# Optimization experiments

Measured on AMD Instinct MI355X. Metric: run time of the kernel, lower is better.

Reference implementation:

```python
import jax, jax.numpy as jnp
import numpy as np

T_HORIZON, S_DIM, A_DIM, H = 65536, 128, 8, 256
GAMMA, LMBDA, EPS_CLIP, VF_COEF, ENT_COEF = 0.99, 0.95, 0.2, 0.5, 0.01
LOG2PI = float(np.log(2.0 * np.pi))


def setup_inputs() -> dict:
    key = jax.random.key(0)
    ks = jax.random.split(key, 24)
    s = jax.random.normal(ks[0], (T_HORIZON, S_DIM), jnp.float32)
    a = jax.random.normal(ks[1], (T_HORIZON, A_DIM), jnp.float32)
    r = jax.random.normal(ks[2], (T_HORIZON, 1), jnp.float32)
    sp = jax.random.normal(ks[3], (T_HORIZON, S_DIM), jnp.float32)
    log_prob_a_old = jax.random.normal(ks[4], (T_HORIZON, 1), jnp.float32)
    d_mask = (jax.random.uniform(ks[5], (T_HORIZON, 1)) > 0.05).astype(jnp.float32)

    def lin(k, fan_in, fan_out, std):
        return jax.random.normal(k, (fan_in, fan_out), jnp.float32) * (std / np.sqrt(fan_in))

    params = dict(
        pi_W1=lin(ks[6], S_DIM, H, np.sqrt(2)), pi_b1=jnp.zeros((H,), jnp.float32),
        pi_W2=lin(ks[7], H, H, np.sqrt(2)),     pi_b2=jnp.zeros((H,), jnp.float32),
        mu_W=lin(ks[8], H, A_DIM, 0.01),        mu_b=jnp.zeros((A_DIM,), jnp.float32),
        log_std=jnp.zeros((A_DIM,), jnp.float32),
        v_W1=lin(ks[9], S_DIM, H, np.sqrt(2)),  v_b1=jnp.zeros((H,), jnp.float32),
        v_W2=lin(ks[10], H, H, np.sqrt(2)),     v_b2=jnp.zeros((H,), jnp.float32),
        vh_W=lin(ks[11], H, 1, 1.0),            vh_b=jnp.zeros((1,), jnp.float32),
    )
    return dict(s=s, a=a, r=r, sp=sp, log_prob_a_old=log_prob_a_old, d_mask=d_mask, **params)


def reference(s, a, r, sp, log_prob_a_old, d_mask,
              pi_W1, pi_b1, pi_W2, pi_b2, mu_W, mu_b, log_std,
              v_W1, v_b1, v_W2, v_b2, vh_W, vh_b):
    def mlp(x, W1, b1, W2, b2):
        return jnp.tanh(jnp.tanh(x @ W1 + b1) @ W2 + b2)

    def v_fn(x):
        return mlp(x, v_W1, v_b1, v_W2, v_b2) @ vh_W + vh_b  # [N, 1]

    # ---- GAE (computed under no_grad in the original) ----
    values = jax.lax.stop_gradient(v_fn(s))                  # [T, 1]
    v_last = jax.lax.stop_gradient(v_fn(sp[-1:]))            # [1, 1]
    next_values = jnp.concatenate([values[1:], v_last], axis=0)
    deltas = r + GAMMA * next_values * d_mask - values       # [T, 1]

    def gae_step(gae, inp):
        delta, m = inp
        gae = delta + GAMMA * LMBDA * m * gae
        return gae, gae

    _, advantages = jax.lax.scan(gae_step, jnp.zeros((1,), deltas.dtype),
                                 (deltas, d_mask), reverse=True)  # [T, 1]
    returns = advantages + values
    advantages = (advantages - advantages.mean()) / (advantages.std(ddof=1) + 1e-8)
    advantages = jax.lax.stop_gradient(advantages)
    returns = jax.lax.stop_gradient(returns)

    # ---- PPO clipped loss (single full-batch pass) ----
    mu = mlp(s, pi_W1, pi_b1, pi_W2, pi_b2) @ mu_W + mu_b    # [T, A]
    std = jnp.exp(log_std)
    log_prob = (-0.5 * ((a - mu) / std) ** 2 - log_std - 0.5 * LOG2PI).sum(-1, keepdims=True)
    ratio = jnp.exp(log_prob - log_prob_a_old)               # [T, 1]
    pg_loss = -jnp.minimum(ratio * advantages,
                           jnp.clip(ratio, 1.0 - EPS_CLIP, 1.0 + EPS_CLIP) * advantages).mean()
    diff = v_fn(s) - returns
    vf_loss = jnp.where(jnp.abs(diff) < 1.0, 0.5 * diff ** 2, jnp.abs(diff) - 0.5).mean()
    entropy = (0.5 + 0.5 * LOG2PI + log_std).mean()          # Normal entropy, constant over batch
    return pg_loss + VF_COEF * vf_loss - ENT_COEF * entropy
```

## Files before the change

kernel.cpp:

```cpp
#include <hip/hip_runtime.h>
#include <math.h>

#define TH 65536
#define SD 128
#define AD 8
#define HD 256

constexpr float GAMMA  = 0.99f;
constexpr float LMBDA  = 0.95f;
constexpr float EPSC   = 0.2f;
constexpr float VFC    = 0.5f;
constexpr float ENTC   = 0.01f;
constexpr float LOG2PI = 1.8378770664093453f;

typedef _Float16 half8 __attribute__((ext_vector_type(8)));
typedef __fp16 fp16x2 __attribute__((ext_vector_type(2)));
typedef __attribute__((ext_vector_type(4))) float f32x4;

constexpr size_t WS_VALUES = 0;
constexpr size_t WS_RATIO  = 131080;
constexpr size_t WS_CHP    = 196616;
constexpr size_t WS_CHB    = 196680;
constexpr size_t WS_SCAL   = 196744;
constexpr size_t WS_BF     = 196752;
constexpr size_t SW_PIW1 = 0;
constexpr size_t SW_PIW2 = 32768;
constexpr size_t SW_VW1  = 98304;
constexpr size_t SW_VW2  = 131072;

__device__ __forceinline__ unsigned pk2h(float a, float b) {
    fp16x2 h = __builtin_amdgcn_cvt_pkrtz(a, b);
    return __builtin_bit_cast(unsigned, h);
}

__device__ __forceinline__ float ftanh(float x) {
    float e = __expf(x + x);
    return fmaf(-2.f, __builtin_amdgcn_rcpf(e + 1.f), 1.f);
}

__device__ __forceinline__ float atomLoad(const float* p) {
    return __hip_atomic_load(p, __ATOMIC_RELAXED, __HIP_MEMORY_SCOPE_AGENT);
}

__global__ __launch_bounds__(256) void swizzle_kernel(
    const float* __restrict__ piW1, const float* __restrict__ vW1,
    const float* __restrict__ piW2, const float* __restrict__ vW2,
    unsigned short* __restrict__ dPiW1, unsigned short* __restrict__ dVW1,
    unsigned short* __restrict__ dPiW2, unsigned short* __restrict__ dVW2,
    float* __restrict__ scal)
{
    if (blockIdx.x == 0 && threadIdx.x < 8) scal[threadIdx.x] = 0.f;
    int g = blockIdx.x * 256 + threadIdx.x;
    const float* S; unsigned short* D; int lo;
    if      (g <  8192) { S = piW1; D = dPiW1; lo = 0;     }
    else if (g < 24576) { S = piW2; D = dPiW2; lo = 8192;  }
    else if (g < 32768) { S = vW1;  D = dVW1;  lo = 24576; }
    else                { S = vW2;  D = dVW2;  lo = 32768; }
    int q = g - lo;
    int k = q >> 6, n4 = (q & 63) * 4;
    float4 v = *(const float4*)(S + (size_t)k * HD + n4);
    int ks = k >> 5, kq = (k >> 3) & 3, j = k & 7;
    int nt = n4 >> 4, nr = n4 & 15;
    unsigned short* base = D + ((size_t)(ks * 16 + nt) * 64 + kq * 16 + nr) * 8 + j;
    unsigned p01 = pk2h(v.x, v.y);
    unsigned p23 = pk2h(v.z, v.w);
    base[0]  = (unsigned short)(p01 & 0xffff);
    base[8]  = (unsigned short)(p01 >> 16);
    base[16] = (unsigned short)(p23 & 0xffff);
    base[24] = (unsigned short)(p23 >> 16);
}

__device__ __forceinline__ void runlayer1(
    f32x4* acc, const unsigned short* __restrict__ Ws,
    const half8* afr, int colhalf, int lane)
{
    const half8* Wp = (const half8*)Ws + (size_t)(colhalf * 8) * 64 + lane;
    half8 b[2][8];
#pragma unroll
    for (int nt = 0; nt < 8; ++nt) acc[nt] = (f32x4){0.f, 0.f, 0.f, 0.f};
#pragma unroll
    for (int nt = 0; nt < 8; ++nt) b[0][nt] = Wp[(0 * 16 + nt) * 64];
#pragma unroll
    for (int nt = 0; nt < 8; ++nt) b[1][nt] = Wp[(1 * 16 + nt) * 64];
#pragma unroll
    for (int ks = 0; ks < 4; ++ks) {
        const int cur = ks & 1;
#pragma unroll
        for (int nt = 0; nt < 8; ++nt)
            acc[nt] = __builtin_amdgcn_mfma_f32_16x16x32_f16(afr[ks], b[cur][nt], acc[nt], 0, 0, 0);
        if (ks < 2) {
#pragma unroll
            for (int nt = 0; nt < 8; ++nt) b[cur][nt] = Wp[((ks + 2) * 16 + nt) * 64];
        }
    }
}

__device__ __forceinline__ void runlayer2(
    f32x4* acc, const unsigned short* __restrict__ Ws,
    const unsigned short* h1, int l15, int quad, int rowgrp, int colhalf, int lane)
{
    const half8* Wp = (const half8*)Ws + (size_t)(colhalf * 8) * 64 + lane;
    const unsigned short* Ap = h1 + (rowgrp * 16 + l15) * 264 + quad * 8;
    half8 b[2][8];
    half8 af[2];
#pragma unroll
    for (int nt = 0; nt < 8; ++nt) acc[nt] = (f32x4){0.f, 0.f, 0.f, 0.f};
    af[0] = *(const half8*)(Ap + 0 * 32);
#pragma unroll
    for (int nt = 0; nt < 8; ++nt) b[0][nt] = Wp[(0 * 16 + nt) * 64];
    af[1] = *(const half8*)(Ap + 1 * 32);
#pragma unroll
    for (int nt = 0; nt < 8; ++nt) b[1][nt] = Wp[(1 * 16 + nt) * 64];
#pragma unroll
    for (int ks = 0; ks < 8; ++ks) {
        const int cur = ks & 1;
#pragma unroll
        for (int nt = 0; nt < 8; ++nt)
            acc[nt] = __builtin_amdgcn_mfma_f32_16x16x32_f16(af[cur], b[cur][nt], acc[nt], 0, 0, 0);
        if (ks < 6) {
            af[cur] = *(const half8*)(Ap + (ks + 2) * 32);
#pragma unroll
            for (int nt = 0; nt < 8; ++nt) b[cur][nt] = Wp[((ks + 2) * 16 + nt) * 64];
        }
    }
}

__device__ __forceinline__ void store4(unsigned short* dst, int stride,
                                       float t0, float t1, float t2, float t3)
{
    unsigned p01 = pk2h(t0, t1), p23 = pk2h(t2, t3);
    dst[0]          = (unsigned short)(p01 & 0xffff);
    dst[stride]     = (unsigned short)(p01 >> 16);
    dst[2 * stride] = (unsigned short)(p23 & 0xffff);
    dst[3 * stride] = (unsigned short)(p23 >> 16);
}

__global__ __launch_bounds__(256, 3) void mlp_fused_kernel(
    const float* __restrict__ X, const float* __restrict__ Xlast,
    const unsigned short* __restrict__ piW1s, const float* __restrict__ pib1,
    const unsigned short* __restrict__ piW2s, const float* __restrict__ pib2,
    const float* __restrict__ muW, const float* __restrict__ mub,
    const float* __restrict__ logstd,
    const float* __restrict__ act, const float* __restrict__ lpold,
    const unsigned short* __restrict__ vW1s, const float* __restrict__ vb1,
    const unsigned short* __restrict__ vW2s, const float* __restrict__ vb2,
    const float* __restrict__ vhW, const float* __restrict__ vhb,
    float* __restrict__ values, float* __restrict__ ratio)
{
    __shared__ unsigned short h1[32 * 264];
    __shared__ float cmb[32 * 8];
    __shared__ float val[32];
    const int tid = threadIdx.x;
    const int lane = tid & 63, wave = tid >> 6;
    const int l15 = lane & 15, quad = lane >> 4;
    const int rowgrp = wave >> 1, colhalf = wave & 1;
    const bool vonly = (blockIdx.x == gridDim.x - 1);
    const float* Xp = vonly ? Xlast : X + (size_t)blockIdx.x * 32 * SD;
    const int nrows = vonly ? 1 : 32;
    const int vout0 = vonly ? TH : blockIdx.x * 32;

    if (tid < 32) val[tid] = 0.f;
    cmb[tid] = 0.f;

    const int rr = rowgrp * 16 + l15;
    const float* xrow = Xp + (size_t)(rr < nrows ? rr : 0) * SD;
    half8 afr[4];
#pragma unroll
    for (int ks = 0; ks < 4; ++ks) {
        float4 v0 = *(const float4*)(xrow + ks * 32 + quad * 8);
        float4 v1 = *(const float4*)(xrow + ks * 32 + quad * 8 + 4);
        if (rr >= nrows) { v0 = make_float4(0.f, 0.f, 0.f, 0.f); v1 = v0; }
        uint4 u = make_uint4(pk2h(v0.x, v0.y), pk2h(v0.z, v0.w),
                             pk2h(v1.x, v1.y), pk2h(v1.z, v1.w));
        afr[ks] = __builtin_bit_cast(half8, u);
    }

    f32x4 acc[8];

    if (!vonly) {
        runlayer1(acc, piW1s, afr, colhalf, lane);
#pragma unroll
        for (int ntl = 0; ntl < 8; ++ntl) {
            int col = (colhalf * 8 + ntl) * 16 + l15;
            float bb = pib1[col];
            store4(&h1[(rowgrp * 16 + quad * 4) * 264 + col], 264,
                   ftanh(acc[ntl][0] + bb), ftanh(acc[ntl][1] + bb),
                   ftanh(acc[ntl][2] + bb), ftanh(acc[ntl][3] + bb));
        }
        __syncthreads();
        runlayer2(acc, piW2s, h1, l15, quad, rowgrp, colhalf, lane);
        float pm[4][8];
#pragma unroll
        for (int rg = 0; rg < 4; ++rg)
#pragma unroll
            for (int aj = 0; aj < 8; ++aj) pm[rg][aj] = 0.f;
#pragma unroll
        for (int ntl = 0; ntl < 8; ++ntl) {
            int col = (colhalf * 8 + ntl) * 16 + l15;
            float bb = pib2[col];
            float4 w0 = *(const float4*)(muW + (size_t)col * AD);
            float4 w1 = *(const float4*)(muW + (size_t)col * AD + 4);
            float wv[8] = {w0.x, w0.y, w0.z, w0.w, w1.x, w1.y, w1.z, w1.w};
#pragma unroll
            for (int rg = 0; rg < 4; ++rg) {
                float hv = ftanh(acc[ntl][rg] + bb);
#pragma unroll
                for (int aj = 0; aj < 8; ++aj) pm[rg][aj] = fmaf(hv, wv[aj], pm[rg][aj]);
            }
        }
#pragma unroll
        for (int off = 8; off >= 1; off >>= 1)
#pragma unroll
            for (int rg = 0; rg < 4; ++rg)
#pragma unroll
                for (int aj = 0; aj < 8; ++aj)
                    pm[rg][aj] += __shfl_xor(pm[rg][aj], off, 16);
        if (l15 == 0) {
#pragma unroll
            for (int rg = 0; rg < 4; ++rg) {
                int rowi = rowgrp * 16 + quad * 4 + rg;
#pragma unroll
                for (int aj = 0; aj < 8; ++aj)
                    atomicAdd(&cmb[rowi * 8 + aj], pm[rg][aj]);
            }
        }
        __syncthreads();
        if (tid < 32) {
            int row = blockIdx.x * 32 + tid;
            const float* ar = act + (size_t)row * AD;
            float lp = 0.f;
#pragma unroll
            for (int aj = 0; aj < 8; ++aj) {
                float ls = logstd[aj];
                float mu = cmb[tid * 8 + aj] + mub[aj];
                float z = (ar[aj] - mu) * __expf(-ls);
                lp += -0.5f * z * z - ls;
            }
            lp -= 4.f * LOG2PI;
            ratio[row] = __expf(lp - lpold[row]);
        }
        __syncthreads();
    }

    runlayer1(acc, vW1s, afr, colhalf, lane);
#pragma unroll
    for (int ntl = 0; ntl < 8; ++ntl) {
        int col = (colhalf * 8 + ntl) * 16 + l15;
        float bb = vb1[col];
        store4(&h1[(rowgrp * 16 + quad * 4) * 264 + col], 264,
               ftanh(acc[ntl][0] + bb), ftanh(acc[ntl][1] + bb),
               ftanh(acc[ntl][2] + bb), ftanh(acc[ntl][3] + bb));
    }
    __syncthreads();
    runlayer2(acc, vW2s, h1, l15, quad, rowgrp, colhalf, lane);
    float vp[4] = {0.f, 0.f, 0.f, 0.f};
#pragma unroll
    for (int ntl = 0; ntl < 8; ++ntl) {
        int col = (colhalf * 8 + ntl) * 16 + l15;
        float bb = vb2[col], w = vhW[col];
#pragma unroll
        for (int rg = 0; rg < 4; ++rg) vp[rg] += ftanh(acc[ntl][rg] + bb) * w;
    }
#pragma unroll
    for (int off = 8; off >= 1; off >>= 1)
#pragma unroll
        for (int rg = 0; rg < 4; ++rg) vp[rg] += __shfl_xor(vp[rg], off, 16);
    if (l15 == 0) {
#pragma unroll
        for (int rg = 0; rg < 4; ++rg)
            atomicAdd(&val[rowgrp * 16 + quad * 4 + rg], vp[rg]);
    }
    __syncthreads();
    if (tid < nrows)
        values[vout0 + tid] = val[tid] + vhb[0];
}

__global__ __launch_bounds__(256) void gae_fused_kernel(
    const float* __restrict__ rw, const float* __restrict__ m,
    const float* __restrict__ values, const float* __restrict__ ratio,
    const float* __restrict__ logstd,
    float* __restrict__ chunkP, float* __restrict__ chunkB,
    float* __restrict__ scal, float* __restrict__ out)
{
    __shared__ float sp_[256], sb_[256];
    __shared__ float cp[64], cb[64];
    __shared__ float red[12];
    __shared__ float bcast[4];
    const int j = threadIdx.x;
    const int t0 = blockIdx.x * 1024 + j * 4;
    const float g = GAMMA * LMBDA;

    float4 vv = *(const float4*)(values + t0);
    float v4 = values[t0 + 4];
    float4 rr = *(const float4*)(rw + t0);
    float4 mm = *(const float4*)(m + t0);
    float vs[5] = {vv.x, vv.y, vv.z, vv.w, v4};
    float rs[4] = {rr.x, rr.y, rr.z, rr.w};
    float ms[4] = {mm.x, mm.y, mm.z, mm.w};
    float ds[4];
#pragma unroll
    for (int i = 0; i < 4; ++i)
        ds[i] = rs[i] + GAMMA * vs[i + 1] * ms[i] - vs[i];

    float P = 1.f, B = 0.f;
#pragma unroll
    for (int i = 3; i >= 0; --i) {
        float p = g * ms[i];
        B = ds[i] + p * B;
        P = p * P;
    }
    sp_[j] = P; sb_[j] = B;
    __syncthreads();
    for (int dstep = 1; dstep < 256; dstep <<= 1) {
        float pj = sp_[j], bj = sb_[j], pk = 1.f, bk = 0.f;
        if (j + dstep < 256) { pk = sp_[j + dstep]; bk = sb_[j + dstep]; }
        __syncthreads();
        sp_[j] = pj * pk;
        sb_[j] = bj + pj * bk;
        __syncthreads();
    }
    if (j == 0) {
        atomicExch(&chunkP[blockIdx.x], sp_[0]);
        atomicExch(&chunkB[blockIdx.x], sb_[0]);
        __threadfence();
        atomicAdd(&scal[5], 1.f);
        while (atomLoad(&scal[5]) < 64.f) __builtin_amdgcn_s_sleep(8);
        __threadfence();
    }
    __syncthreads();
    if (j < 64) {
        cp[j] = atomLoad(&chunkP[j]);
        cb[j] = atomLoad(&chunkB[j]);
    }
    __syncthreads();
    if (j == 0) {
        float A = 0.f;
        for (int c = 63; c > (int)blockIdx.x; --c) A = cb[c] + cp[c] * A;
        bcast[0] = A;
    }
    __syncthreads();
    const float carry = bcast[0];

    float Pe = 1.f, Be = 0.f;
    if (j < 255) { Pe = sp_[j + 1]; Be = sb_[j + 1]; }
    float A = Be + Pe * carry;
    float s1 = 0.f, s2 = 0.f, vf = 0.f;
    float a4[4];
#pragma unroll
    for (int i = 3; i >= 0; --i) {
        A = ds[i] + g * ms[i] * A;
        a4[i] = A;
        float ab = fabsf(A);
        vf += (ab < 1.f) ? 0.5f * A * A : ab - 0.5f;
        s1 += A;
        s2 += A * A;
    }
#pragma unroll
    for (int off = 32; off >= 1; off >>= 1) {
        s1 += __shfl_down(s1, off, 64);
        s2 += __shfl_down(s2, off, 64);
        vf += __shfl_down(vf, off, 64);
    }
    if ((j & 63) == 0) {
        int w = j >> 6;
        red[w] = s1; red[4 + w] = s2; red[8 + w] = vf;
    }
    __syncthreads();
    if (j == 0) {
        atomicAdd(&scal[0], red[0] + red[1] + red[2] + red[3]);
        atomicAdd(&scal[1], red[4] + red[5] + red[6] + red[7]);
        atomicAdd(&scal[2], red[8] + red[9] + red[10] + red[11]);
        __threadfence();
        atomicAdd(&scal[6], 1.f);
        while (atomLoad(&scal[6]) < 64.f) __builtin_amdgcn_s_sleep(8);
        __threadfence();
        bcast[1] = atomLoad(&scal[0]);
        bcast[2] = atomLoad(&scal[1]);
    }
    __syncthreads();

    const float ssum = bcast[1], ssq = bcast[2];
    const float meanA = ssum / (float)TH;
    const float varA = fmaxf((ssq - ssum * ssum / (float)TH) / (float)(TH - 1), 0.f);
    const float inv = 1.f / (sqrtf(varA) + 1e-8f);

    float4 r4 = *(const float4*)(ratio + t0);
    float rt[4] = {r4.x, r4.y, r4.z, r4.w};
    float pg = 0.f;
#pragma unroll
    for (int i = 0; i < 4; ++i) {
        float aN = (a4[i] - meanA) * inv;
        float rc = fminf(fmaxf(rt[i], 1.f - EPSC), 1.f + EPSC);
        pg -= fminf(rt[i] * aN, rc * aN);
    }
#pragma unroll
    for (int off = 32; off >= 1; off >>= 1) pg += __shfl_down(pg, off, 64);
    if ((j & 63) == 0) red[j >> 6] = pg;
    __syncthreads();
    if (j == 0) {
        atomicAdd(&scal[3], red[0] + red[1] + red[2] + red[3]);
        __threadfence();
        float old = atomicAdd(&scal[4], 1.f);
        if (old == 63.f) {
            float pgs = atomLoad(&scal[3]);
            float vfs = atomLoad(&scal[2]);
            float ls = 0.f;
#pragma unroll
            for (int jj = 0; jj < AD; ++jj) ls += logstd[jj];
            float entropy = 0.5f + 0.5f * LOG2PI + ls / (float)AD;
            out[0] = pgs / (float)TH + VFC * (vfs / (float)TH) - ENTC * entropy;
        }
    }
}

extern "C" void kernel_launch(void* const* d_in, const int* in_sizes, int n_in,
                              void* d_out, int out_size, void* d_ws, size_t ws_size,
                              hipStream_t stream) {
    const float* s      = (const float*)d_in[0];
    const float* a      = (const float*)d_in[1];
    const float* r      = (const float*)d_in[2];
    const float* sp     = (const float*)d_in[3];
    const float* lpold  = (const float*)d_in[4];
    const float* dmask  = (const float*)d_in[5];
    const float* piW1   = (const float*)d_in[6];
    const float* pib1   = (const float*)d_in[7];
    const float* piW2   = (const float*)d_in[8];
    const float* pib2   = (const float*)d_in[9];
    const float* muW    = (const float*)d_in[10];
    const float* mub    = (const float*)d_in[11];
    const float* logstd = (const float*)d_in[12];
    const float* vW1    = (const float*)d_in[13];
    const float* vb1    = (const float*)d_in[14];
    const float* vW2    = (const float*)d_in[15];
    const float* vb2    = (const float*)d_in[16];
    const float* vhW    = (const float*)d_in[17];
    const float* vhb    = (const float*)d_in[18];

    float* ws      = (float*)d_ws;
    float* values  = ws + WS_VALUES;
    float* ratio   = ws + WS_RATIO;
    float* chunkP  = ws + WS_CHP;
    float* chunkB  = ws + WS_CHB;
    float* scal    = ws + WS_SCAL;
    unsigned short* bfbase = (unsigned short*)(ws + WS_BF);
    unsigned short* dPiW1 = bfbase + SW_PIW1;
    unsigned short* dPiW2 = bfbase + SW_PIW2;
    unsigned short* dVW1  = bfbase + SW_VW1;
    unsigned short* dVW2  = bfbase + SW_VW2;

    swizzle_kernel<<<192, 256, 0, stream>>>(piW1, vW1, piW2, vW2,
                                            dPiW1, dVW1, dPiW2, dVW2, scal);

    mlp_fused_kernel<<<TH / 32 + 1, 256, 0, stream>>>(
        s, sp + (size_t)(TH - 1) * SD,
        dPiW1, pib1, dPiW2, pib2, muW, mub, logstd, a, lpold,
        dVW1, vb1, dVW2, vb2, vhW, vhb,
        values, ratio);

    gae_fused_kernel<<<64, 256, 0, stream>>>(r, dmask, values, ratio, logstd,
                                             chunkP, chunkB, scal, (float*)d_out);
}
```

Measured before the change: 216.9 us.

## Split fused GAE kernel into three launches replacing grid spin barriers

Replaces the single GAE kernel, which used atomic counters and spin-waits as grid-wide barriers, with three separate kernels: chunk scan, carry plus moment sums, and final normalization plus policy loss. Each later kernel recomputes the block-local scan instead of keeping it across a barrier. Per-block partial sums go to workspace arrays instead of float atomics, which also makes the reductions deterministic. The cost is two extra kernel launches and repeated loads and scans of the values, rewards and mask.

```diff
diff --git a/kernel.cpp b/kernel.cpp
--- a/kernel.cpp
+++ b/kernel.cpp
@@ -27,6 +27,10 @@
 constexpr size_t SW_PIW2 = 32768;
 constexpr size_t SW_VW1  = 98304;
 constexpr size_t SW_VW2  = 131072;
+constexpr size_t WS_S1P  = 295056;
+constexpr size_t WS_S2P  = 295120;
+constexpr size_t WS_VFP  = 295184;
+constexpr size_t WS_PGP  = 295248;
 
 __device__ __forceinline__ unsigned pk2h(float a, float b) {
     fp16x2 h = __builtin_amdgcn_cvt_pkrtz(a, b);
@@ -275,29 +279,19 @@
         values[vout0 + tid] = val[tid] + vhb[0];
 }
 
-__global__ __launch_bounds__(256) void gae_fused_kernel(
+__device__ __forceinline__ void gae_block_scan(
     const float* __restrict__ rw, const float* __restrict__ m,
-    const float* __restrict__ values, const float* __restrict__ ratio,
-    const float* __restrict__ logstd,
-    float* __restrict__ chunkP, float* __restrict__ chunkB,
-    float* __restrict__ scal, float* __restrict__ out)
-{
-    __shared__ float sp_[256], sb_[256];
-    __shared__ float cp[64], cb[64];
-    __shared__ float red[12];
-    __shared__ float bcast[4];
-    const int j = threadIdx.x;
-    const int t0 = blockIdx.x * 1024 + j * 4;
-    const float g = GAMMA * LMBDA;
-
+    const float* __restrict__ values, int t0, int j,
+    float* sp_, float* sb_, float* ds, float* ms)
+{
     float4 vv = *(const float4*)(values + t0);
     float v4 = values[t0 + 4];
     float4 rr = *(const float4*)(rw + t0);
     float4 mm = *(const float4*)(m + t0);
     float vs[5] = {vv.x, vv.y, vv.z, vv.w, v4};
     float rs[4] = {rr.x, rr.y, rr.z, rr.w};
-    float ms[4] = {mm.x, mm.y, mm.z, mm.w};
-    float ds[4];
+    ms[0] = mm.x; ms[1] = mm.y; ms[2] = mm.z; ms[3] = mm.w;
+    const float g = GAMMA * LMBDA;
 #pragma unroll
     for (int i = 0; i < 4; ++i)
         ds[i] = rs[i] + GAMMA * vs[i + 1] * ms[i] - vs[i];
@@ -319,37 +313,58 @@
         sb_[j] = bj + pj * bk;
         __syncthreads();
     }
-    if (j == 0) {
-        atomicExch(&chunkP[blockIdx.x], sp_[0]);
-        atomicExch(&chunkB[blockIdx.x], sb_[0]);
-        __threadfence();
-        atomicAdd(&scal[5], 1.f);
-        while (atomLoad(&scal[5]) < 64.f) __builtin_amdgcn_s_sleep(8);
-        __threadfence();
-    }
-    __syncthreads();
-    if (j < 64) {
-        cp[j] = atomLoad(&chunkP[j]);
-        cb[j] = atomLoad(&chunkB[j]);
-    }
+}
+
+__device__ __forceinline__ float gae_carry(
+    const float* __restrict__ chunkP, const float* __restrict__ chunkB,
+    int j, int bid, float* cp, float* cb, float* bcast)
+{
+    if (j < 64) { cp[j] = chunkP[j]; cb[j] = chunkB[j]; }
     __syncthreads();
     if (j == 0) {
         float A = 0.f;
-        for (int c = 63; c > (int)blockIdx.x; --c) A = cb[c] + cp[c] * A;
+        for (int c = 63; c > bid; --c) A = cb[c] + cp[c] * A;
         bcast[0] = A;
     }
     __syncthreads();
-    const float carry = bcast[0];
+    return bcast[0];
+}
+
+__global__ __launch_bounds__(256) void gae_scan_kernel(
+    const float* __restrict__ rw, const float* __restrict__ m,
+    const float* __restrict__ values,
+    float* __restrict__ chunkP, float* __restrict__ chunkB)
+{
+    __shared__ float sp_[256], sb_[256];
+    const int j = threadIdx.x;
+    float ds[4], ms[4];
+    gae_block_scan(rw, m, values, blockIdx.x * 1024 + j * 4, j, sp_, sb_, ds, ms);
+    if (j == 0) { chunkP[blockIdx.x] = sp_[0]; chunkB[blockIdx.x] = sb_[0]; }
+}
+
+__global__ __launch_bounds__(256) void gae_mid_kernel(
+    const float* __restrict__ rw, const float* __restrict__ m,
+    const float* __restrict__ values,
+    const float* __restrict__ chunkP, const float* __restrict__ chunkB,
+    float* __restrict__ s1p, float* __restrict__ s2p, float* __restrict__ vfp)
+{
+    __shared__ float sp_[256], sb_[256];
+    __shared__ float cp[64], cb[64];
+    __shared__ float red[12];
+    __shared__ float bcast[1];
+    const int j = threadIdx.x;
+    const float g = GAMMA * LMBDA;
+    float ds[4], ms[4];
+    gae_block_scan(rw, m, values, blockIdx.x * 1024 + j * 4, j, sp_, sb_, ds, ms);
+    const float carry = gae_carry(chunkP, chunkB, j, blockIdx.x, cp, cb, bcast);
 
     float Pe = 1.f, Be = 0.f;
     if (j < 255) { Pe = sp_[j + 1]; Be = sb_[j + 1]; }
     float A = Be + Pe * carry;
     float s1 = 0.f, s2 = 0.f, vf = 0.f;
-    float a4[4];
 #pragma unroll
     for (int i = 3; i >= 0; --i) {
         A = ds[i] + g * ms[i] * A;
-        a4[i] = A;
         float ab = fabsf(A);
         vf += (ab < 1.f) ? 0.5f * A * A : ab - 0.5f;
         s1 += A;
@@ -367,22 +382,57 @@
     }
     __syncthreads();
     if (j == 0) {
-        atomicAdd(&scal[0], red[0] + red[1] + red[2] + red[3]);
-        atomicAdd(&scal[1], red[4] + red[5] + red[6] + red[7]);
-        atomicAdd(&scal[2], red[8] + red[9] + red[10] + red[11]);
-        __threadfence();
-        atomicAdd(&scal[6], 1.f);
-        while (atomLoad(&scal[6]) < 64.f) __builtin_amdgcn_s_sleep(8);
-        __threadfence();
-        bcast[1] = atomLoad(&scal[0]);
-        bcast[2] = atomLoad(&scal[1]);
-    }
-    __syncthreads();
-
-    const float ssum = bcast[1], ssq = bcast[2];
+        s1p[blockIdx.x] = red[0] + red[1] + red[2] + red[3];
+        s2p[blockIdx.x] = red[4] + red[5] + red[6] + red[7];
+        vfp[blockIdx.x] = red[8] + red[9] + red[10] + red[11];
+    }
+}
+
+__global__ __launch_bounds__(256) void gae_fin_kernel(
+    const float* __restrict__ rw, const float* __restrict__ m,
+    const float* __restrict__ values, const float* __restrict__ ratio,
+    const float* __restrict__ logstd,
+    const float* __restrict__ chunkP, const float* __restrict__ chunkB,
+    const float* __restrict__ s1p, const float* __restrict__ s2p,
+    const float* __restrict__ vfp,
+    float* __restrict__ pgp, float* __restrict__ scal, float* __restrict__ out)
+{
+    __shared__ float sp_[256], sb_[256];
+    __shared__ float cp[64], cb[64];
+    __shared__ float red[4];
+    __shared__ float bcast[4];
+    const int j = threadIdx.x;
+    const int t0 = blockIdx.x * 1024 + j * 4;
+    const float g = GAMMA * LMBDA;
+    float ds[4], ms[4];
+    gae_block_scan(rw, m, values, t0, j, sp_, sb_, ds, ms);
+    const float carry = gae_carry(chunkP, chunkB, j, blockIdx.x, cp, cb, bcast);
+
+    if (j < 64) {
+        float a = s1p[j], b = s2p[j], c = vfp[j];
+#pragma unroll
+        for (int off = 32; off >= 1; off >>= 1) {
+            a += __shfl_down(a, off, 64);
+            b += __shfl_down(b, off, 64);
+            c += __shfl_down(c, off, 64);
+        }
+        if (j == 0) { bcast[1] = a; bcast[2] = b; bcast[3] = c; }
+    }
+    __syncthreads();
+    const float ssum = bcast[1], ssq = bcast[2], vfs = bcast[3];
     const float meanA = ssum / (float)TH;
     const float varA = fmaxf((ssq - ssum * ssum / (float)TH) / (float)(TH - 1), 0.f);
     const float inv = 1.f / (sqrtf(varA) + 1e-8f);
+
+    float Pe = 1.f, Be = 0.f;
+    if (j < 255) { Pe = sp_[j + 1]; Be = sb_[j + 1]; }
+    float A = Be + Pe * carry;
+    float a4[4];
+#pragma unroll
+    for (int i = 3; i >= 0; --i) {
+        A = ds[i] + g * ms[i] * A;
+        a4[i] = A;
+    }
 
     float4 r4 = *(const float4*)(ratio + t0);
     float rt[4] = {r4.x, r4.y, r4.z, r4.w};
@@ -398,12 +448,12 @@
     if ((j & 63) == 0) red[j >> 6] = pg;
     __syncthreads();
     if (j == 0) {
-        atomicAdd(&scal[3], red[0] + red[1] + red[2] + red[3]);
+        pgp[blockIdx.x] = red[0] + red[1] + red[2] + red[3];
         __threadfence();
         float old = atomicAdd(&scal[4], 1.f);
         if (old == 63.f) {
-            float pgs = atomLoad(&scal[3]);
-            float vfs = atomLoad(&scal[2]);
+            float pgs = 0.f;
+            for (int c = 0; c < 64; ++c) pgs += atomLoad(&pgp[c]);
             float ls = 0.f;
 #pragma unroll
             for (int jj = 0; jj < AD; ++jj) ls += logstd[jj];
@@ -442,6 +492,10 @@
     float* chunkP  = ws + WS_CHP;
     float* chunkB  = ws + WS_CHB;
     float* scal    = ws + WS_SCAL;
+    float* s1p     = ws + WS_S1P;
+    float* s2p     = ws + WS_S2P;
+    float* vfp     = ws + WS_VFP;
+    float* pgp     = ws + WS_PGP;
     unsigned short* bfbase = (unsigned short*)(ws + WS_BF);
     unsigned short* dPiW1 = bfbase + SW_PIW1;
     unsigned short* dPiW2 = bfbase + SW_PIW2;
@@ -457,6 +511,10 @@
         dVW1, vb1, dVW2, vb2, vhW, vhb,
         values, ratio);
 
-    gae_fused_kernel<<<64, 256, 0, stream>>>(r, dmask, values, ratio, logstd,
-                                             chunkP, chunkB, scal, (float*)d_out);
-}
+    gae_scan_kernel<<<64, 256, 0, stream>>>(r, dmask, values, chunkP, chunkB);
+    gae_mid_kernel<<<64, 256, 0, stream>>>(r, dmask, values, chunkP, chunkB,
+                                           s1p, s2p, vfp);
+    gae_fin_kernel<<<64, 256, 0, stream>>>(r, dmask, values, ratio, logstd,
+                                           chunkP, chunkB, s1p, s2p, vfp,
+                                           pgp, scal, (float*)d_out);
+}
```

Measured after the change: 211.5 us. 1.03x faster.
